# Kernel tuning notes

Hardware: AMD Instinct MI355X
Metric: run time of the kernel (lower is better)

## Reference

```python
import jax, jax.numpy as jnp
import numpy as np
import math

E = 1024      # embed_dim
H = 16        # num_heads
D = 32        # head_dim = E // H // 2
DEPTH = 12
LAMBDA_INIT = 0.8 - 0.6 * math.exp(-0.3 * DEPTH)
B, T = 4, 1024
EPS = 1e-5


def setup_inputs() -> dict:
    key = jax.random.key(0)
    ks = jax.random.split(key, 10)
    s = 0.02  # realistic init scale for weight matrices
    return {
        "x": jax.random.normal(ks[0], (B, T, E), jnp.float32),
        "Wq": jax.random.normal(ks[1], (E, E), jnp.float32) * s,
        "Wk": jax.random.normal(ks[2], (E, E), jnp.float32) * s,
        "Wv": jax.random.normal(ks[3], (E, E), jnp.float32) * s,
        "Wo": jax.random.normal(ks[4], (E, E), jnp.float32) * s,
        "lambda_q1": jax.random.normal(ks[5], (D,), jnp.float32) * 0.1,
        "lambda_k1": jax.random.normal(ks[6], (D,), jnp.float32) * 0.1,
        "lambda_q2": jax.random.normal(ks[7], (D,), jnp.float32) * 0.1,
        "lambda_k2": jax.random.normal(ks[8], (D,), jnp.float32) * 0.1,
        "g": jnp.ones((2 * D,), jnp.float32),  # subln affine weight
    }


def reference(x, Wq, Wk, Wv, Wo, lambda_q1, lambda_k1, lambda_q2, lambda_k2, g):
    b, t, _ = x.shape
    scaling = D ** -0.5
    # projections (torch Linear: x @ W.T), split into 2H half-width q/k heads
    q = (x @ Wq.T).reshape(b, t, 2 * H, D).transpose(0, 2, 1, 3) * scaling  # [b,2H,t,D]
    k = (x @ Wk.T).reshape(b, t, 2 * H, D).transpose(0, 2, 1, 3)            # [b,2H,t,D]
    v = (x @ Wv.T).reshape(b, t, H, 2 * D).transpose(0, 2, 1, 3)            # [b,H,t,2D]
    # dual score maps, fp32 softmax
    aw = jnp.einsum('bhqd,bhkd->bhqk', q, k)               # [b,2H,t,t]
    aw = jnp.nan_to_num(aw)
    aw = jax.nn.softmax(aw.astype(jnp.float32), axis=-1).astype(q.dtype)
    # scalar lambda
    lam1 = jnp.exp(jnp.sum(lambda_q1 * lambda_k1))
    lam2 = jnp.exp(jnp.sum(lambda_q2 * lambda_k2))
    lam = lam1 - lam2 + LAMBDA_INIT
    # differential subtract of the paired softmax maps
    aw = aw.reshape(b, H, 2, t, t)
    aw = aw[:, :, 0] - lam * aw[:, :, 1]                   # [b,H,t,t]
    attn = jnp.einsum('bhqk,bhkd->bhqd', aw, v)            # [b,H,t,2D]
    # per-head RMSNorm over 2D channel dim (affine)
    attn = attn * jax.lax.rsqrt(jnp.mean(attn * attn, axis=-1, keepdims=True) + EPS) * g
    attn = attn * (1.0 - LAMBDA_INIT)
    attn = attn.transpose(0, 2, 1, 3).reshape(b, t, H * 2 * D)  # [b,t,E]
    return attn @ Wo.T
```

## Files before the change

### kernel.cpp

```cpp
#include <hip/hip_runtime.h>
#include <math.h>

#define E_   1024
#define H_   16
#define B_   4
#define T_   1024
#define LAMBDA_INIT 0.783605766532f
#define SCALE_Q 0.17677669529663687f

typedef short s16x8 __attribute__((ext_vector_type(8)));
typedef float f32x4 __attribute__((ext_vector_type(4)));

__device__ inline ushort f2bf(float x) {
    unsigned u = __builtin_bit_cast(unsigned, x);
    u += 0x7fffu + ((u >> 16) & 1u);
    return (ushort)(u >> 16);
}

__device__ inline void gl_lds16(const ushort* g, ushort* l) {
    __builtin_amdgcn_global_load_lds((const __attribute__((address_space(1))) void*)g,
                                     (__attribute__((address_space(3))) void*)l,
                                     16, 0, 0);
}

__global__ __launch_bounds__(256) void cast_x(const float* __restrict__ in,
                                              ushort* __restrict__ out)
{
    int i = (blockIdx.x * 256 + threadIdx.x) * 8;
    float4 a = *(const float4*)&in[i];
    float4 b = *(const float4*)&in[i + 4];
    union { ushort u[8]; uint4 v; } o;
    o.u[0] = f2bf(a.x); o.u[1] = f2bf(a.y); o.u[2] = f2bf(a.z); o.u[3] = f2bf(a.w);
    o.u[4] = f2bf(b.x); o.u[5] = f2bf(b.y); o.u[6] = f2bf(b.z); o.u[7] = f2bf(b.w);
    *(uint4*)&out[i] = o.v;
}

__global__ __launch_bounds__(256) void cast_w4(
    const float* __restrict__ w0, const float* __restrict__ w1,
    const float* __restrict__ w2, const float* __restrict__ w3,
    ushort* __restrict__ o0, ushort* __restrict__ o1,
    ushort* __restrict__ o2, ushort* __restrict__ o3)
{
    const float* in = blockIdx.y == 0 ? w0 : (blockIdx.y == 1 ? w1 : (blockIdx.y == 2 ? w2 : w3));
    ushort* out = blockIdx.y == 0 ? o0 : (blockIdx.y == 1 ? o1 : (blockIdx.y == 2 ? o2 : o3));
    int i = (blockIdx.x * 256 + threadIdx.x) * 8;
    float4 a = *(const float4*)&in[i];
    float4 b = *(const float4*)&in[i + 4];
    union { ushort u[8]; uint4 v; } o;
    o.u[0] = f2bf(a.x); o.u[1] = f2bf(a.y); o.u[2] = f2bf(a.z); o.u[3] = f2bf(a.w);
    o.u[4] = f2bf(b.x); o.u[5] = f2bf(b.y); o.u[6] = f2bf(b.z); o.u[7] = f2bf(b.w);
    *(uint4*)&out[i] = o.v;
}

__global__ void lam_kernel(const float* __restrict__ lq1, const float* __restrict__ lk1,
                           const float* __restrict__ lq2, const float* __restrict__ lk2,
                           float* __restrict__ lamp)
{
    int l = threadIdx.x;
    float p1 = 0.f, p2 = 0.f;
    if (l < 32) { p1 = lq1[l] * lk1[l]; p2 = lq2[l] * lk2[l]; }
    #pragma unroll
    for (int off = 32; off; off >>= 1) {
        p1 += __shfl_xor(p1, off);
        p2 += __shfl_xor(p2, off);
    }
    if (l == 0) lamp[0] = expf(p1) - expf(p2) + LAMBDA_INIT;
}

__global__ __launch_bounds__(256) void gemm_qkv(
    const ushort* __restrict__ Xb, const ushort* __restrict__ Wqb,
    const ushort* __restrict__ Wkb, const ushort* __restrict__ Wvb,
    ushort* __restrict__ QKV)
{
    __shared__ ushort As[128 * 32];
    __shared__ ushort Ws[128 * 32];
    const int tid = threadIdx.x;
    const int wave = tid >> 6, lane = tid & 63;
    const int l15 = lane & 15, quad = lane >> 4;
    const int bm = blockIdx.y * 128;
    const int bng = blockIdx.x * 128;
    const int region = bng >> 10;
    const ushort* W = region == 0 ? Wqb : (region == 1 ? Wkb : Wvb);
    const float scale = region == 0 ? SCALE_Q : 1.0f;
    const int wn = bng & 1023;
    const int lrow = lane >> 2;
    const int lcol = (lane & 3) * 8;

    f32x4 acc[4][4] = {};
    const int wr = wave >> 1, wc = wave & 1;

    for (int k0 = 0; k0 < 1024; k0 += 32) {
        #pragma unroll
        for (int p = 0; p < 2; ++p) {
            int i = wave + 4 * p;
            gl_lds16(&Xb[(size_t)(bm + i * 16 + lrow) * 1024 + k0 + lcol], &As[i * 512]);
            gl_lds16(&W [(size_t)(wn + i * 16 + lrow) * 1024 + k0 + lcol], &Ws[i * 512]);
        }
        __syncthreads();
        s16x8 a[4], b[4];
        #pragma unroll
        for (int i = 0; i < 4; ++i)
            a[i] = *(const s16x8*)&As[(wr * 64 + i * 16 + l15) * 32 + quad * 8];
        #pragma unroll
        for (int j = 0; j < 4; ++j)
            b[j] = *(const s16x8*)&Ws[(wc * 64 + j * 16 + l15) * 32 + quad * 8];
        #pragma unroll
        for (int i = 0; i < 4; ++i)
            #pragma unroll
            for (int j = 0; j < 4; ++j)
                acc[i][j] = __builtin_amdgcn_mfma_f32_16x16x32_bf16(a[i], b[j], acc[i][j], 0, 0, 0);
        __syncthreads();
    }

    #pragma unroll
    for (int i = 0; i < 4; ++i)
        #pragma unroll
        for (int j = 0; j < 4; ++j)
            #pragma unroll
            for (int r = 0; r < 4; ++r) {
                int row = bm + wr * 64 + i * 16 + quad * 4 + r;
                int col = bng + wc * 64 + j * 16 + l15;
                QKV[(size_t)row * 3072 + col] = f2bf(acc[i][j][r] * scale);
            }
}

__global__ __launch_bounds__(256) void gemm_out(
    const ushort* __restrict__ Ab, const ushort* __restrict__ Wob,
    float* __restrict__ C)
{
    __shared__ ushort As[64 * 32];
    __shared__ ushort Ws[128 * 32];
    const int tid = threadIdx.x;
    const int wave = tid >> 6, lane = tid & 63;
    const int l15 = lane & 15, quad = lane >> 4;
    const int bm = blockIdx.y * 64;
    const int bn = blockIdx.x * 128;
    const int lrow = lane >> 2;
    const int lcol = (lane & 3) * 8;

    f32x4 acc[2][4] = {};
    const int wr = wave >> 1, wc = wave & 1;

    for (int k0 = 0; k0 < 1024; k0 += 32) {
        gl_lds16(&Ab[(size_t)(bm + wave * 16 + lrow) * 1024 + k0 + lcol], &As[wave * 512]);
        #pragma unroll
        for (int p = 0; p < 2; ++p) {
            int i = wave + 4 * p;
            gl_lds16(&Wob[(size_t)(bn + i * 16 + lrow) * 1024 + k0 + lcol], &Ws[i * 512]);
        }
        __syncthreads();
        s16x8 a[2], b[4];
        #pragma unroll
        for (int i = 0; i < 2; ++i)
            a[i] = *(const s16x8*)&As[(wr * 32 + i * 16 + l15) * 32 + quad * 8];
        #pragma unroll
        for (int j = 0; j < 4; ++j)
            b[j] = *(const s16x8*)&Ws[(wc * 64 + j * 16 + l15) * 32 + quad * 8];
        #pragma unroll
        for (int i = 0; i < 2; ++i)
            #pragma unroll
            for (int j = 0; j < 4; ++j)
                acc[i][j] = __builtin_amdgcn_mfma_f32_16x16x32_bf16(a[i], b[j], acc[i][j], 0, 0, 0);
        __syncthreads();
    }

    #pragma unroll
    for (int i = 0; i < 2; ++i)
        #pragma unroll
        for (int j = 0; j < 4; ++j)
            #pragma unroll
            for (int r = 0; r < 4; ++r) {
                int row = bm + wr * 32 + i * 16 + quad * 4 + r;
                int col = bn + wc * 64 + j * 16 + l15;
                C[(size_t)row * 1024 + col] = acc[i][j][r];
            }
}

__global__ __launch_bounds__(256) void transpose_v(
    const ushort* __restrict__ QKV, ushort* __restrict__ Vt)
{
    __shared__ ushort Ls[64][72];
    const int tid = threadIdx.x;
    const int m0 = blockIdx.x * 64;
    const int b  = m0 >> 10;
    const int t0 = m0 & 1023;
    const int e0 = blockIdx.y * 64;
    #pragma unroll
    for (int p = 0; p < 2; ++p) {
        int idx = tid + 256 * p;
        int r = idx >> 3, seg = (idx & 7) * 8;
        *(uint4*)&Ls[r][seg] =
            *(const uint4*)&QKV[(size_t)(m0 + r) * 3072 + 2048 + e0 + seg];
    }
    __syncthreads();
    #pragma unroll
    for (int p = 0; p < 2; ++p) {
        int idx = tid + 256 * p;
        int er = idx >> 3, ts = (idx & 7) * 8;
        union { ushort u[8]; uint4 v; } o;
        #pragma unroll
        for (int i = 0; i < 8; ++i) o.u[i] = Ls[ts + i][er];
        *(uint4*)&Vt[((size_t)b * E_ + e0 + er) * T_ + t0 + ts] = o.v;
    }
}

__global__ __launch_bounds__(256) void diff_attn(
    const ushort* __restrict__ QKV, const ushort* __restrict__ Vt,
    const float* __restrict__ g, const float* __restrict__ lamp,
    ushort* __restrict__ O)
{
    __shared__ __align__(16) ushort Qs[64][72];
    __shared__ __align__(16) ushort Ks[64][72];
    __shared__ __align__(16) ushort Vts[64][72];
    __shared__ __align__(16) ushort Ps[4][16][68];

    const int tid  = threadIdx.x;
    const int lane = tid & 63;
    const int wave = tid >> 6;
    const int l15  = lane & 15;
    const int quad = lane >> 4;

    const int blk = blockIdx.x;
    const int qt = blk & 15;
    const int h  = (blk >> 4) & 15;
    const int b  = blk >> 8;
    const int q0 = qt * 64;
    const int hoff = h * 64;
    const size_t rowbase = (size_t)b * T_;
    const size_t vtbase = ((size_t)b * E_ + hoff) * T_;

    const ushort* Qg = QKV;
    const ushort* Kg = QKV + 1024;

    #pragma unroll
    for (int p = 0; p < 2; ++p) {
        int idx = tid + 256 * p;
        int r = idx >> 3, seg = (idx & 7) * 8;
        *(uint4*)&Qs[r][seg] =
            *(const uint4*)&Qg[(rowbase + q0 + r) * 3072 + hoff + seg];
    }
    const float lam = lamp[0];
    float gv[4];
    #pragma unroll
    for (int j = 0; j < 4; ++j) gv[j] = g[j * 16 + l15];
    __syncthreads();

    s16x8 aq[2];
    #pragma unroll
    for (int c = 0; c < 2; ++c)
        aq[c] = *(const s16x8*)&Qs[wave * 16 + l15][c * 32 + quad * 8];

    const f32x4 zf = {0.f, 0.f, 0.f, 0.f};
    f32x4 o0[4] = {zf, zf, zf, zf};
    f32x4 o1[4] = {zf, zf, zf, zf};
    float lsum[2][4] = {};

    for (int kt = 0; kt < T_ / 64; ++kt) {
        __syncthreads();
        #pragma unroll
        for (int p = 0; p < 2; ++p) {
            int idx = tid + 256 * p;
            int r = idx >> 3, seg = (idx & 7) * 8;
            *(uint4*)&Ks[r][seg] =
                *(const uint4*)&Kg[(rowbase + kt * 64 + r) * 3072 + hoff + seg];
            *(uint4*)&Vts[r][seg] =
                *(const uint4*)&Vt[vtbase + (size_t)r * T_ + kt * 64 + seg];
        }
        __syncthreads();

        s16x8 bk0[4], bk1[4], vt0[4], vt1[4];
        #pragma unroll
        for (int j = 0; j < 4; ++j) {
            bk0[j] = *(const s16x8*)&Ks [j * 16 + l15][     quad * 8];
            bk1[j] = *(const s16x8*)&Ks [j * 16 + l15][32 + quad * 8];
            vt0[j] = *(const s16x8*)&Vts[j * 16 + l15][     quad * 8];
            vt1[j] = *(const s16x8*)&Vts[j * 16 + l15][32 + quad * 8];
        }

        #pragma unroll
        for (int c = 0; c < 2; ++c) {
            f32x4 S[4];
            #pragma unroll
            for (int j = 0; j < 4; ++j)
                S[j] = __builtin_amdgcn_mfma_f32_16x16x32_bf16(
                    aq[c], c ? bk1[j] : bk0[j], zf, 0, 0, 0);
            #pragma unroll
            for (int j = 0; j < 4; ++j)
                #pragma unroll
                for (int r = 0; r < 4; ++r) {
                    float e = __expf(S[j][r]);
                    lsum[c][r] += e;
                    Ps[wave][quad * 4 + r][j * 16 + l15] = f2bf(e);
                }
            s16x8 pa0 = *(const s16x8*)&Ps[wave][l15][     quad * 8];
            s16x8 pa1 = *(const s16x8*)&Ps[wave][l15][32 + quad * 8];
            f32x4* oc = c ? o1 : o0;
            #pragma unroll
            for (int j = 0; j < 4; ++j) {
                oc[j] = __builtin_amdgcn_mfma_f32_16x16x32_bf16(pa0, vt0[j], oc[j], 0, 0, 0);
                oc[j] = __builtin_amdgcn_mfma_f32_16x16x32_bf16(pa1, vt1[j], oc[j], 0, 0, 0);
            }
        }
    }

    #pragma unroll
    for (int c = 0; c < 2; ++c)
        #pragma unroll
        for (int r = 0; r < 4; ++r) {
            float s = lsum[c][r];
            s += __shfl_xor(s, 1); s += __shfl_xor(s, 2);
            s += __shfl_xor(s, 4); s += __shfl_xor(s, 8);
            lsum[c][r] = s;
        }

    float val[4][4];
    float ssq[4] = {0.f, 0.f, 0.f, 0.f};
    #pragma unroll
    for (int r = 0; r < 4; ++r) {
        float i0 = 1.f / lsum[0][r];
        float i1 = lam / lsum[1][r];
        #pragma unroll
        for (int j = 0; j < 4; ++j) {
            float v = o0[j][r] * i0 - o1[j][r] * i1;
            val[j][r] = v;
            ssq[r] += v * v;
        }
    }
    #pragma unroll
    for (int r = 0; r < 4; ++r) {
        float s = ssq[r];
        s += __shfl_xor(s, 1); s += __shfl_xor(s, 2);
        s += __shfl_xor(s, 4); s += __shfl_xor(s, 8);
        ssq[r] = rsqrtf(s * (1.f / 64.f) + 1e-5f);
    }
    const float fin = 1.f - LAMBDA_INIT;
    #pragma unroll
    for (int r = 0; r < 4; ++r)
        #pragma unroll
        for (int j = 0; j < 4; ++j)
            O[(rowbase + q0 + wave * 16 + quad * 4 + r) * 1024 + hoff + j * 16 + l15]
                = f2bf(val[j][r] * ssq[r] * gv[j] * fin);
}

extern "C" void kernel_launch(void* const* d_in, const int* in_sizes, int n_in,
                              void* d_out, int out_size, void* d_ws, size_t ws_size,
                              hipStream_t stream)
{
    const float* x   = (const float*)d_in[0];
    const float* Wq  = (const float*)d_in[1];
    const float* Wk  = (const float*)d_in[2];
    const float* Wv  = (const float*)d_in[3];
    const float* Wo  = (const float*)d_in[4];
    const float* lq1 = (const float*)d_in[5];
    const float* lk1 = (const float*)d_in[6];
    const float* lq2 = (const float*)d_in[7];
    const float* lk2 = (const float*)d_in[8];
    const float* g   = (const float*)d_in[9];
    float* out = (float*)d_out;

    const int M = B_ * T_;
    const size_t ME = (size_t)M * E_;
    const size_t EE = (size_t)E_ * E_;
    ushort* xb  = (ushort*)d_ws;
    ushort* Wqb = xb  + ME;
    ushort* Wkb = Wqb + EE;
    ushort* Wvb = Wkb + EE;
    ushort* Wob = Wvb + EE;
    ushort* QKV = Wob + EE;
    ushort* Vtb = QKV + (size_t)M * 3072;
    ushort* Ab  = Vtb + ME;
    float*  lamp = (float*)(Ab + ME);

    cast_x<<<ME / (256 * 8), 256, 0, stream>>>(x, xb);
    cast_w4<<<dim3(EE / (256 * 8), 4), 256, 0, stream>>>(Wq, Wk, Wv, Wo, Wqb, Wkb, Wvb, Wob);
    lam_kernel<<<1, 64, 0, stream>>>(lq1, lk1, lq2, lk2, lamp);
    gemm_qkv<<<dim3(24, 32), 256, 0, stream>>>(xb, Wqb, Wkb, Wvb, QKV);
    transpose_v<<<dim3(M / 64, E_ / 64), 256, 0, stream>>>(QKV, Vtb);
    diff_attn<<<B_ * H_ * (T_ / 64), 256, 0, stream>>>(QKV, Vtb, g, lamp, Ab);
    gemm_out<<<dim3(8, 64), 256, 0, stream>>>(Ab, Wob, out);
}
```

Baseline: 220.5 us.

## Double query rows per attention block and compute transposed scores for lane-local row sums

Each attention block now handles 128 query rows instead of 64, with each wave owning two 16-row tiles, so every K/V tile loaded into shared memory is reused across twice as many queries and the grid is halved. The score and PV MFMAs swap operand order so each lane holds one query row, which turns the row-sum and RMSNorm reductions into two cross-quad shuffles and allows packed bf16 conversion and stores. The Q staging buffer is reused as per-wave P scratch. This raises register pressure from the doubled accumulators, and with half as many blocks occupancy may drop.

```diff
diff --git a/kernel.cpp b/kernel.cpp
--- a/kernel.cpp
+++ b/kernel.cpp
@@ -15,6 +15,20 @@
     unsigned u = __builtin_bit_cast(unsigned, x);
     u += 0x7fffu + ((u >> 16) & 1u);
     return (ushort)(u >> 16);
+}
+
+__device__ inline uint f2bf2(float lo, float hi) {
+#if __has_builtin(__builtin_amdgcn_cvt_pk_bf16_f32)
+    typedef __bf16 bf16x2_t __attribute__((ext_vector_type(2)));
+    bf16x2_t r = __builtin_amdgcn_cvt_pk_bf16_f32(lo, hi);
+    return __builtin_bit_cast(uint, r);
+#else
+    uint ul = __builtin_bit_cast(uint, lo);
+    uint uh = __builtin_bit_cast(uint, hi);
+    ul += 0x7fffu + ((ul >> 16) & 1u);
+    uh += 0x7fffu + ((uh >> 16) & 1u);
+    return __builtin_amdgcn_perm(uh, ul, 0x07060302u);
+#endif
 }
 
 __device__ inline void gl_lds16(const ushort* g, ushort* l) {
@@ -209,10 +223,9 @@
     const float* __restrict__ g, const float* __restrict__ lamp,
     ushort* __restrict__ O)
 {
-    __shared__ __align__(16) ushort Qs[64][72];
     __shared__ __align__(16) ushort Ks[64][72];
     __shared__ __align__(16) ushort Vts[64][72];
-    __shared__ __align__(16) ushort Ps[4][16][68];
+    __shared__ __align__(16) ushort QP[9216];
 
     const int tid  = threadIdx.x;
     const int lane = tid & 63;
@@ -221,10 +234,10 @@
     const int quad = lane >> 4;
 
     const int blk = blockIdx.x;
-    const int qt = blk & 15;
-    const int h  = (blk >> 4) & 15;
-    const int b  = blk >> 8;
-    const int q0 = qt * 64;
+    const int qt = blk & 7;
+    const int h  = (blk >> 3) & 15;
+    const int b  = blk >> 7;
+    const int q0 = qt * 128;
     const int hoff = h * 64;
     const size_t rowbase = (size_t)b * T_;
     const size_t vtbase = ((size_t)b * E_ + hoff) * T_;
@@ -233,27 +246,34 @@
     const ushort* Kg = QKV + 1024;
 
     #pragma unroll
-    for (int p = 0; p < 2; ++p) {
+    for (int p = 0; p < 4; ++p) {
         int idx = tid + 256 * p;
         int r = idx >> 3, seg = (idx & 7) * 8;
-        *(uint4*)&Qs[r][seg] =
+        *(uint4*)&QP[r * 72 + seg] =
             *(const uint4*)&Qg[(rowbase + q0 + r) * 3072 + hoff + seg];
     }
     const float lam = lamp[0];
-    float gv[4];
-    #pragma unroll
-    for (int j = 0; j < 4; ++j) gv[j] = g[j * 16 + l15];
+    float4 gv[4];
+    #pragma unroll
+    for (int jt = 0; jt < 4; ++jt) gv[jt] = *(const float4*)&g[jt * 16 + quad * 4];
     __syncthreads();
 
-    s16x8 aq[2];
+    s16x8 aq[2][2];
     #pragma unroll
     for (int c = 0; c < 2; ++c)
-        aq[c] = *(const s16x8*)&Qs[wave * 16 + l15][c * 32 + quad * 8];
+        #pragma unroll
+        for (int rt = 0; rt < 2; ++rt)
+            aq[c][rt] = *(const s16x8*)&QP[(wave * 32 + rt * 16 + l15) * 72 + c * 32 + quad * 8];
 
     const f32x4 zf = {0.f, 0.f, 0.f, 0.f};
-    f32x4 o0[4] = {zf, zf, zf, zf};
-    f32x4 o1[4] = {zf, zf, zf, zf};
-    float lsum[2][4] = {};
+    f32x4 o[2][2][4];
+    #pragma unroll
+    for (int c = 0; c < 2; ++c)
+        #pragma unroll
+        for (int rt = 0; rt < 2; ++rt)
+            #pragma unroll
+            for (int jt = 0; jt < 4; ++jt) o[c][rt][jt] = zf;
+    float lsum[2][2] = {};
 
     for (int kt = 0; kt < T_ / 64; ++kt) {
         __syncthreads();
@@ -268,37 +288,49 @@
         }
         __syncthreads();
 
-        s16x8 bk0[4], bk1[4], vt0[4], vt1[4];
-        #pragma unroll
-        for (int j = 0; j < 4; ++j) {
-            bk0[j] = *(const s16x8*)&Ks [j * 16 + l15][     quad * 8];
-            bk1[j] = *(const s16x8*)&Ks [j * 16 + l15][32 + quad * 8];
-            vt0[j] = *(const s16x8*)&Vts[j * 16 + l15][     quad * 8];
-            vt1[j] = *(const s16x8*)&Vts[j * 16 + l15][32 + quad * 8];
-        }
+        s16x8 va[4][2];
+        #pragma unroll
+        for (int jt = 0; jt < 4; ++jt)
+            #pragma unroll
+            for (int h2 = 0; h2 < 2; ++h2)
+                va[jt][h2] = *(const s16x8*)&Vts[jt * 16 + l15][h2 * 32 + quad * 8];
 
         #pragma unroll
         for (int c = 0; c < 2; ++c) {
-            f32x4 S[4];
-            #pragma unroll
-            for (int j = 0; j < 4; ++j)
-                S[j] = __builtin_amdgcn_mfma_f32_16x16x32_bf16(
-                    aq[c], c ? bk1[j] : bk0[j], zf, 0, 0, 0);
-            #pragma unroll
-            for (int j = 0; j < 4; ++j)
+            s16x8 ka[4];
+            #pragma unroll
+            for (int jk = 0; jk < 4; ++jk)
+                ka[jk] = *(const s16x8*)&Ks[jk * 16 + l15][c * 32 + quad * 8];
+
+            #pragma unroll
+            for (int rt = 0; rt < 2; ++rt) {
+                ushort* Pt = &QP[(wave * 2 + rt) * 1152];
+                f32x4 S[4];
                 #pragma unroll
-                for (int r = 0; r < 4; ++r) {
-                    float e = __expf(S[j][r]);
-                    lsum[c][r] += e;
-                    Ps[wave][quad * 4 + r][j * 16 + l15] = f2bf(e);
+                for (int jk = 0; jk < 4; ++jk)
+                    S[jk] = __builtin_amdgcn_mfma_f32_16x16x32_bf16(ka[jk], aq[c][rt], zf, 0, 0, 0);
+                float part = 0.f;
+                #pragma unroll
+                for (int jk = 0; jk < 4; ++jk) {
+                    float e0 = __expf(S[jk][0]);
+                    float e1 = __expf(S[jk][1]);
+                    float e2 = __expf(S[jk][2]);
+                    float e3 = __expf(S[jk][3]);
+                    part += (e0 + e1) + (e2 + e3);
+                    uint2 pk;
+                    pk.x = f2bf2(e0, e1);
+                    pk.y = f2bf2(e2, e3);
+                    *(uint2*)&Pt[l15 * 72 + jk * 16 + quad * 4] = pk;
                 }
-            s16x8 pa0 = *(const s16x8*)&Ps[wave][l15][     quad * 8];
-            s16x8 pa1 = *(const s16x8*)&Ps[wave][l15][32 + quad * 8];
-            f32x4* oc = c ? o1 : o0;
-            #pragma unroll
-            for (int j = 0; j < 4; ++j) {
-                oc[j] = __builtin_amdgcn_mfma_f32_16x16x32_bf16(pa0, vt0[j], oc[j], 0, 0, 0);
-                oc[j] = __builtin_amdgcn_mfma_f32_16x16x32_bf16(pa1, vt1[j], oc[j], 0, 0, 0);
+                lsum[c][rt] += part;
+                #pragma unroll
+                for (int h2 = 0; h2 < 2; ++h2) {
+                    s16x8 pf = *(const s16x8*)&Pt[l15 * 72 + h2 * 32 + quad * 8];
+                    #pragma unroll
+                    for (int jt = 0; jt < 4; ++jt)
+                        o[c][rt][jt] = __builtin_amdgcn_mfma_f32_16x16x32_bf16(
+                            va[jt][h2], pf, o[c][rt][jt], 0, 0, 0);
+                }
             }
         }
     }
@@ -306,40 +338,41 @@
     #pragma unroll
     for (int c = 0; c < 2; ++c)
         #pragma unroll
-        for (int r = 0; r < 4; ++r) {
-            float s = lsum[c][r];
-            s += __shfl_xor(s, 1); s += __shfl_xor(s, 2);
-            s += __shfl_xor(s, 4); s += __shfl_xor(s, 8);
-            lsum[c][r] = s;
-        }
-
-    float val[4][4];
-    float ssq[4] = {0.f, 0.f, 0.f, 0.f};
-    #pragma unroll
-    for (int r = 0; r < 4; ++r) {
-        float i0 = 1.f / lsum[0][r];
-        float i1 = lam / lsum[1][r];
-        #pragma unroll
-        for (int j = 0; j < 4; ++j) {
-            float v = o0[j][r] * i0 - o1[j][r] * i1;
-            val[j][r] = v;
-            ssq[r] += v * v;
-        }
-    }
-    #pragma unroll
-    for (int r = 0; r < 4; ++r) {
-        float s = ssq[r];
-        s += __shfl_xor(s, 1); s += __shfl_xor(s, 2);
-        s += __shfl_xor(s, 4); s += __shfl_xor(s, 8);
-        ssq[r] = rsqrtf(s * (1.f / 64.f) + 1e-5f);
-    }
+        for (int rt = 0; rt < 2; ++rt) {
+            float s = lsum[c][rt];
+            s += __shfl_xor(s, 16);
+            s += __shfl_xor(s, 32);
+            lsum[c][rt] = s;
+        }
+
     const float fin = 1.f - LAMBDA_INIT;
     #pragma unroll
-    for (int r = 0; r < 4; ++r)
-        #pragma unroll
-        for (int j = 0; j < 4; ++j)
-            O[(rowbase + q0 + wave * 16 + quad * 4 + r) * 1024 + hoff + j * 16 + l15]
-                = f2bf(val[j][r] * ssq[r] * gv[j] * fin);
+    for (int rt = 0; rt < 2; ++rt) {
+        float i0 = 1.f / lsum[0][rt];
+        float i1 = lam / lsum[1][rt];
+        float val[4][4];
+        float ssq = 0.f;
+        #pragma unroll
+        for (int jt = 0; jt < 4; ++jt)
+            #pragma unroll
+            for (int r = 0; r < 4; ++r) {
+                float v = o[0][rt][jt][r] * i0 - o[1][rt][jt][r] * i1;
+                val[jt][r] = v;
+                ssq += v * v;
+            }
+        ssq += __shfl_xor(ssq, 16);
+        ssq += __shfl_xor(ssq, 32);
+        float sc = rsqrtf(ssq * (1.f / 64.f) + 1e-5f) * fin;
+        size_t rowoff = (rowbase + q0 + wave * 32 + rt * 16 + l15) * 1024 + hoff;
+        #pragma unroll
+        for (int jt = 0; jt < 4; ++jt) {
+            float gx = gv[jt].x, gy = gv[jt].y, gz = gv[jt].z, gw = gv[jt].w;
+            uint p01 = f2bf2(val[jt][0] * sc * gx, val[jt][1] * sc * gy);
+            uint p23 = f2bf2(val[jt][2] * sc * gz, val[jt][3] * sc * gw);
+            *(uint*)&O[rowoff + jt * 16 + quad * 4 + 0] = p01;
+            *(uint*)&O[rowoff + jt * 16 + quad * 4 + 2] = p23;
+        }
+    }
 }
 
 extern "C" void kernel_launch(void* const* d_in, const int* in_sizes, int n_in,
@@ -376,6 +409,6 @@
     lam_kernel<<<1, 64, 0, stream>>>(lq1, lk1, lq2, lk2, lamp);
     gemm_qkv<<<dim3(24, 32), 256, 0, stream>>>(xb, Wqb, Wkb, Wvb, QKV);
     transpose_v<<<dim3(M / 64, E_ / 64), 256, 0, stream>>>(QKV, Vtb);
-    diff_attn<<<B_ * H_ * (T_ / 64), 256, 0, stream>>>(QKV, Vtb, g, lamp, Ab);
+    diff_attn<<<B_ * H_ * (T_ / 128), 256, 0, stream>>>(QKV, Vtb, g, lamp, Ab);
     gemm_out<<<dim3(8, 64), 256, 0, stream>>>(Ab, Wob, out);
 }
```

Result: no change. 223.1 us (+1.2%).
